# Kernel optimization log

Measured on AMD Instinct MI355X. Metric: run time of the kernel, lower is better.

The kernel has to match this reference:

```python
import jax, jax.numpy as jnp
import numpy as np

B, T = 128, 50
VOCAB, EMB_D, GRU_H = 10000, 200, 100
HEADS, AHID, THID = 8, 96, 96

def _conv(x, w, b, pad):
    y = jax.lax.conv_general_dilated(x, w, (1, 1), pad,
        dimension_numbers=('NCHW', 'OIHW', 'NCHW'))
    return y + b[None, :, None, None]

def _bn(x, g, b, m, v):
    s = jax.lax.rsqrt(v + 1e-5)
    return (x - m[None, :, None, None]) * (g * s)[None, :, None, None] + b[None, :, None, None]

def _maxpool(x):
    return jax.lax.reduce_window(x, -jnp.inf, jax.lax.max, (1, 1, 2, 2), (1, 1, 2, 2), 'VALID')

def _resize(x):
    # F.interpolate(mode='bilinear', align_corners=False) == half-pixel bilinear, no antialias
    return jax.image.resize(x, (x.shape[0], x.shape[1], 25, 156), 'bilinear', antialias=False)

def _audio_attn(x, wq, bq, wk, bk, wv, bv):
    # x: [B,96,H,W]; wq: [heads,96,96] == stacked per-head 1x1 convs
    Q = jnp.einsum('bchw,noc->bnohw', x, wq) + bq[None, :, :, None, None]
    K = jnp.einsum('bchw,noc->bnohw', x, wk) + bk[None, :, :, None, None]
    V = jnp.einsum('bchw,noc->bnohw', x, wv) + bv[None, :, :, None, None]
    # torch F.softmax with no dim on a 4D tensor defaults to dim=1 (channels) -> axis=2 here
    return jax.nn.softmax(Q * K, axis=2) * V  # [B,heads,96,H,W]

def _text_attn(o, wq, bq, wk, bk, wv, bv):
    # o: [N,100]; wq: [heads,96,100] == stacked per-head Linear layers
    Q = jnp.einsum('nd,hod->nho', o, wq) + bq[None]
    K = jnp.einsum('nd,hod->nho', o, wk) + bk[None]
    V = jnp.einsum('nd,hod->nho', o, wv) + bv[None]
    a = jax.nn.softmax(Q * K, axis=2) * V  # 2D softmax default dim=1 -> over feature axis
    return a.reshape(o.shape[0], -1)  # head-concat order == torch cat along dim=1

def _gru(xs, w_ih, w_hh, b_ih, b_hh):
    # xs: [T,B,200]; torch gate order r, z, n; b_hn applied inside r-gating
    def step(h, x):
        gi = x @ w_ih.T + b_ih
        gh = h @ w_hh.T + b_hh
        ir, iz, inew = jnp.split(gi, 3, axis=1)
        hr, hz, hnew = jnp.split(gh, 3, axis=1)
        r = jax.nn.sigmoid(ir + hr)
        z = jax.nn.sigmoid(iz + hz)
        n = jnp.tanh(inew + r * hnew)
        h2 = (1.0 - z) * n + z * h
        return h2, h2
    h0 = jnp.zeros((xs.shape[1], GRU_H), xs.dtype)
    hT, outs = jax.lax.scan(step, h0, xs)
    return outs, hT

def _forward(tokens, lengths, mfcc_t, mfcc_f, mfcc_c, w1a, b1a, g1a, be1a, m1a, v1a, w1b, b1b, g1b, be1b, m1b, v1b, w2, b2, g2, be2, m2, v2, w3, b3, g3, be3, m3, v3, w4, b4, g4, be4, m4, v4, wq_a1, bq_a1, wk_a1, bk_a1, wv_a1, bv_a1, wq_a2, bq_a2, wk_a2, bk_a2, wv_a2, bv_a2, emb, w_ih, w_hh, b_ih, b_hh, wq_t1, bq_t1, wk_t1, bk_t1, wv_t1, bv_t1, wq_t2, bq_t2, wk_t2, bk_t2, wv_t2, bv_t2, w_fa, b_fa, w_ft, b_ft, w_e, b_e):
    # --- audio CNN stem (eval-mode batchnorm; dropout off) ---
    xa = jax.nn.relu(_bn(_conv(mfcc_t, w1a, b1a, 'VALID'), g1a, be1a, m1a, v1a))
    xb = jax.nn.relu(_bn(_conv(mfcc_f, w1b, b1b, 'VALID'), g1b, be1b, m1b, v1b))
    # NOTE: original source reuses conv1b/bn1b for the third input (faithful to that)
    xc = jax.nn.relu(_bn(_conv(mfcc_c, w1b, b1b, 'VALID'), g1b, be1b, m1b, v1b))
    x = jnp.concatenate([_resize(xa), _resize(xb), _resize(xc)], axis=1)  # [B,24,25,156]
    x = _maxpool(jax.nn.relu(_bn(_conv(x, w2, b2, [(1, 1), (1, 1)]), g2, be2, m2, v2)))  # [B,32,12,78]
    x = _maxpool(jax.nn.relu(_bn(_conv(x, w3, b3, [(1, 1), (1, 1)]), g3, be3, m3, v3)))  # [B,64,6,39]
    x = jax.nn.relu(_bn(_conv(x, w4, b4, [(1, 1), (1, 1)]), g4, be4, m4, v4))            # [B,96,6,39]
    # --- two stacked per-head audio attentions, then per-head spatial GAP ---
    a1 = _audio_attn(x, wq_a1, bq_a1, wk_a1, bk_a1, wv_a1, bv_a1).mean(axis=(-2, -1))  # [B,8,96]
    a2 = _audio_attn(x, wq_a2, bq_a2, wk_a2, bk_a2, wv_a2, bv_a2).mean(axis=(-2, -1))
    # forward() slices heads along the height concat and GAPs -> per head [stage1 96, stage2 96]
    self_attn_audio = jnp.concatenate([a1, a2], axis=2).reshape(x.shape[0], -1)  # [B,1536]
    # --- text branch: embedding + GRU (all lengths == T -> pack/pad is identity) ---
    ex = jnp.swapaxes(emb[tokens], 0, 1)  # [T,B,200]
    outs, h = _gru(ex, w_ih, w_hh, b_ih, b_hh)  # h: [B,100]
    output = jnp.swapaxes(outs, 0, 1).reshape(-1, GRU_H)  # [B*T,100]
    t1 = _text_attn(output, wq_t1, bq_t1, wk_t1, bk_t1, wv_t1, bv_t1)
    t2 = _text_attn(output, wq_t2, bq_t2, wk_t2, bk_t2, wv_t2, bv_t2)
    self_attn_text = jnp.concatenate([t1, t2], axis=1).reshape(x.shape[0], T, -1).sum(axis=1)  # [B,1536]
    # --- cross-modal gated fusion ---
    x_gap = x.mean(axis=(-2, -1))  # [B,96]
    a_text = jax.nn.softmax(x_gap @ w_fa.T + b_fa, axis=1)   # [B,100]
    attn_text_based_audio = a_text * h                        # [B,100]
    a_audio = jax.nn.softmax(h @ w_ft.T + b_ft, axis=1)      # [B,96]
    attn_audio_based_text = a_audio * x_gap                   # [B,96]
    feat = jnp.concatenate([self_attn_audio, self_attn_text,
                            attn_audio_based_text, attn_text_based_audio], axis=1)  # [B,3268]
    return feat @ w_e.T + b_e  # [B,4] emotion logits

def setup_inputs() -> dict:
    key = jax.random.key(0)
    ks = iter(jax.random.split(key, 100))
    nrm = lambda s, sc=0.05: jax.random.normal(next(ks), s, jnp.float32) * sc
    uni = lambda s: jax.random.uniform(next(ks), s, jnp.float32) * 0.5 + 0.5
    d = {}
    d['mfcc_t'] = jax.random.normal(next(ks), (B, 1, 200, 40), jnp.float32)
    d['mfcc_f'] = jax.random.normal(next(ks), (B, 1, 200, 40), jnp.float32)
    d['mfcc_c'] = jax.random.normal(next(ks), (B, 1, 200, 40), jnp.float32)
    d['tokens'] = jax.random.randint(next(ks), (B, T), 0, VOCAB)
    d['lengths'] = jnp.full((B,), T, jnp.int32)
    def bnp(pre, c):
        d['g' + pre] = 1.0 + nrm((c,)); d['be' + pre] = nrm((c,))
        d['m' + pre] = nrm((c,)); d['v' + pre] = uni((c,))
    d['w1a'] = nrm((8, 1, 5, 2), 0.2); d['b1a'] = nrm((8,)); bnp('1a', 8)
    d['w1b'] = nrm((8, 1, 2, 6), 0.2); d['b1b'] = nrm((8,)); bnp('1b', 8)
    d['w2'] = nrm((32, 24, 3, 3), 0.1); d['b2'] = nrm((32,)); bnp('2', 32)
    d['w3'] = nrm((64, 32, 3, 3), 0.1); d['b3'] = nrm((64,)); bnp('3', 64)
    d['w4'] = nrm((96, 64, 3, 3), 0.08); d['b4'] = nrm((96,)); bnp('4', 96)
    for s in ('1', '2'):
        for p in ('q', 'k', 'v'):
            d['w%s_a%s' % (p, s)] = nrm((HEADS, 96, 96), 0.1)
            d['b%s_a%s' % (p, s)] = nrm((HEADS, 96))
    d['emb'] = nrm((VOCAB, EMB_D), 0.1)
    d['w_ih'] = nrm((3 * GRU_H, EMB_D), 0.1); d['w_hh'] = nrm((3 * GRU_H, GRU_H), 0.1)
    d['b_ih'] = nrm((3 * GRU_H,)); d['b_hh'] = nrm((3 * GRU_H,))
    for s in ('1', '2'):
        for p in ('q', 'k', 'v'):
            d['w%s_t%s' % (p, s)] = nrm((HEADS, THID, GRU_H), 0.1)
            d['b%s_t%s' % (p, s)] = nrm((HEADS, THID))
    d['w_fa'] = nrm((100, 96), 0.1); d['b_fa'] = nrm((100,))
    d['w_ft'] = nrm((96, 100), 0.1); d['b_ft'] = nrm((96,))
    d['w_e'] = nrm((4, 2 * HEADS * AHID + 2 * HEADS * THID + 96 + 100), 0.05); d['b_e'] = nrm((4,))
    return d

def reference(mfcc_t, mfcc_f, mfcc_c, tokens, lengths, w1a, b1a, g1a, be1a, m1a, v1a, w1b, b1b, g1b, be1b, m1b, v1b, w2, b2, g2, be2, m2, v2, w3, b3, g3, be3, m3, v3, w4, b4, g4, be4, m4, v4, wq_a1, bq_a1, wk_a1, bk_a1, wv_a1, bv_a1, wq_a2, bq_a2, wk_a2, bk_a2, wv_a2, bv_a2, emb, w_ih, w_hh, b_ih, b_hh, wq_t1, bq_t1, wk_t1, bk_t1, wv_t1, bv_t1, wq_t2, bq_t2, wk_t2, bk_t2, wv_t2, bv_t2, w_fa, b_fa, w_ft, b_ft, w_e, b_e):
    return _forward(tokens, lengths, mfcc_t, mfcc_f, mfcc_c, w1a, b1a, g1a, be1a, m1a, v1a, w1b, b1b, g1b, be1b, m1b, v1b, w2, b2, g2, be2, m2, v2, w3, b3, g3, be3, m3, v3, w4, b4, g4, be4, m4, v4, wq_a1, bq_a1, wk_a1, bk_a1, wv_a1, bv_a1, wq_a2, bq_a2, wk_a2, bk_a2, wv_a2, bv_a2, emb, w_ih, w_hh, b_ih, b_hh, wq_t1, bq_t1, wk_t1, bk_t1, wv_t1, bv_t1, wq_t2, bq_t2, wk_t2, bk_t2, wv_t2, bv_t2, w_fa, b_fa, w_ft, b_ft, w_e, b_e)
```

## Files before the change

### kernel.cpp

```cpp
#include <hip/hip_runtime.h>
#include <math.h>

static constexpr int kB = 128;
static constexpr int kT = 50;

struct TDesc { const float* src; float* dst; int O; int C; int total; };
struct TPack { TDesc d[15]; };
__global__ void k_transpose_pack(TPack p, float* __restrict__ za) {
    if (blockIdx.y == 15) {
        for (int i = blockIdx.x * 256 + threadIdx.x; i < 196608; i += 76800)
            za[i] = 0.f;
        return;
    }
    TDesc t = p.d[blockIdx.y];
    int idx = blockIdx.x * 256 + threadIdx.x;
    if (idx >= t.total) return;
    int o = idx % t.O; int r = idx / t.O; int c = r % t.C; int n = r / t.C;
    t.dst[idx] = t.src[((size_t)n * t.O + o) * t.C + c];
}

__global__ void __launch_bounds__(320) k_gi(const int* __restrict__ tokens,
        const float* __restrict__ emb, const float* __restrict__ w_ih,
        const float* __restrict__ b_ih, float* __restrict__ GI) {
    int r0 = blockIdx.x * 8;
    int tid = threadIdx.x;
    __shared__ float er[8][200];
    for (int e = tid; e < 1600; e += 320) {
        int r = e / 200, c = e - r * 200;
        er[r][c] = emb[(size_t)tokens[r0 + r] * 200 + c];
    }
    __syncthreads();
    if (tid < 300) {
        float acc[8];
        float bv = b_ih[tid];
        #pragma unroll
        for (int r = 0; r < 8; ++r) acc[r] = bv;
        for (int k4 = 0; k4 < 50; ++k4) {
            float4 w4 = *(const float4*)(w_ih + (size_t)tid * 200 + k4 * 4);
            #pragma unroll
            for (int r = 0; r < 8; ++r) {
                float4 x4 = *(const float4*)&er[r][k4 * 4];
                acc[r] += w4.x * x4.x + w4.y * x4.y + w4.z * x4.z + w4.w * x4.w;
            }
        }
        #pragma unroll
        for (int r = 0; r < 8; ++r)
            GI[(size_t)(r0 + r) * 300 + tid] = acc[r];
    }
}

__global__ void __launch_bounds__(256) k_fat_stem_gru(
    const float* __restrict__ mt, const float* __restrict__ mf,
    const float* __restrict__ mc,
    const float* __restrict__ w1a, const float* __restrict__ b1a,
    const float* __restrict__ g1a, const float* __restrict__ be1a,
    const float* __restrict__ m1a, const float* __restrict__ v1a,
    const float* __restrict__ w1b, const float* __restrict__ b1b,
    const float* __restrict__ g1b, const float* __restrict__ be1b,
    const float* __restrict__ m1b, const float* __restrict__ v1b,
    float* __restrict__ out, int total,
    const float* __restrict__ GI, const float* __restrict__ w_hh,
    const float* __restrict__ b_hh, float* __restrict__ outsT) {
    if (blockIdx.x < 128) {
        const int b = blockIdx.x, tid = threadIdx.x;
        __shared__ float hs[100];
        __shared__ float gH[300];
        const float bias0 = b_hh[tid];
        const float bias1 = (tid < 44) ? b_hh[256 + tid] : 0.f;
        if (tid < 100) hs[tid] = 0.f;
        __syncthreads();
        for (int t = 0; t < kT; ++t) {
            {
                float gh = bias0;
                const float* wr = w_hh + (size_t)tid * 100;
                #pragma unroll
                for (int k4 = 0; k4 < 25; ++k4) {
                    float4 w4 = *(const float4*)(wr + k4 * 4);
                    float4 h4 = *(const float4*)&hs[k4 * 4];
                    gh += w4.x * h4.x + w4.y * h4.y + w4.z * h4.z + w4.w * h4.w;
                }
                gH[tid] = gh;
            }
            if (tid < 44) {
                float gh = bias1;
                const float* wr = w_hh + (size_t)(256 + tid) * 100;
                #pragma unroll
                for (int k4 = 0; k4 < 25; ++k4) {
                    float4 w4 = *(const float4*)(wr + k4 * 4);
                    float4 h4 = *(const float4*)&hs[k4 * 4];
                    gh += w4.x * h4.x + w4.y * h4.y + w4.z * h4.z + w4.w * h4.w;
                }
                gH[256 + tid] = gh;
            }
            __syncthreads();
            if (tid < 100) {
                const float* gi = GI + ((size_t)b * kT + t) * 300;
                float r = 1.f / (1.f + expf(-(gi[tid] + gH[tid])));
                float z = 1.f / (1.f + expf(-(gi[100 + tid] + gH[100 + tid])));
                float nn = tanhf(gi[200 + tid] + r * gH[200 + tid]);
                float h2 = (1.f - z) * nn + z * hs[tid];
                hs[tid] = h2;
                outsT[((size_t)b * 100 + tid) * kT + t] = h2;
            }
            __syncthreads();
        }
        return;
    }
    int idx = (blockIdx.x - 128) * 256 + threadIdx.x;
    if (idx >= total) return;
    int ox = idx % 156; int t = idx / 156;
    int oy = t % 25; t /= 25;
    int ch = t % 24; int b = t / 24;
    int grp = ch >> 3, c = ch & 7;
    const float* src; int Hc, Wc;
    const float *wb, *cb, *g, *be, *m, *v;
    if (grp == 0) { src = mt; Hc = 196; Wc = 39; wb = w1a + c * 10;
                    cb = b1a; g = g1a; be = be1a; m = m1a; v = v1a; }
    else          { src = (grp == 1 ? mf : mc); Hc = 199; Wc = 35; wb = w1b + c * 12;
                    cb = b1b; g = g1b; be = be1b; m = m1b; v = v1b; }
    float s = g[c] * rsqrtf(v[c] + 1e-5f);
    float bias = (cb[c] - m[c]) * s + be[c];
    float sy = (oy + 0.5f) * ((float)Hc / 25.f) - 0.5f;
    float sx = (ox + 0.5f) * ((float)Wc / 156.f) - 0.5f;
    float fy0 = floorf(sy), fx0 = floorf(sx);
    float fy = sy - fy0, fx = sx - fx0;
    int y0 = (int)fy0, x0 = (int)fx0;
    int y0c = min(max(y0, 0), Hc - 1), y1c = min(max(y0 + 1, 0), Hc - 1);
    int x0c = min(max(x0, 0), Wc - 1), x1c = min(max(x0 + 1, 0), Wc - 1);
    bool xs = (x1c == x0c), ys = (y1c == y0c);
    const float* p = src + (size_t)b * 8000;
    float t00, t01, t10, t11;
    if (grp == 0) {
        float W[6][3];
        #pragma unroll
        for (int r = 0; r < 6; ++r) {
            int rr = min(y0c + r, 199);
            #pragma unroll
            for (int cc = 0; cc < 3; ++cc)
                W[r][cc] = p[rr * 40 + min(x0c + cc, 39)];
        }
        float a00 = 0.f, a01 = 0.f, a10 = 0.f, a11 = 0.f;
        #pragma unroll
        for (int ky = 0; ky < 5; ++ky)
            #pragma unroll
            for (int kx = 0; kx < 2; ++kx) {
                float wv = wb[ky * 2 + kx];
                a00 += W[ky][kx] * wv;     a01 += W[ky][kx + 1] * wv;
                a10 += W[ky + 1][kx] * wv; a11 += W[ky + 1][kx + 1] * wv;
            }
        t00 = a00;
        t01 = xs ? a00 : a01;
        t10 = ys ? a00 : a10;
        t11 = xs ? (ys ? a00 : a10) : (ys ? a01 : a11);
    } else {
        float W[3][7];
        #pragma unroll
        for (int r = 0; r < 3; ++r) {
            int rr = min(y0c + r, 199);
            #pragma unroll
            for (int cc = 0; cc < 7; ++cc)
                W[r][cc] = p[rr * 40 + min(x0c + cc, 39)];
        }
        float a00 = 0.f, a01 = 0.f, a10 = 0.f, a11 = 0.f;
        #pragma unroll
        for (int ky = 0; ky < 2; ++ky)
            #pragma unroll
            for (int kx = 0; kx < 6; ++kx) {
                float wv = wb[ky * 6 + kx];
                a00 += W[ky][kx] * wv;     a01 += W[ky][kx + 1] * wv;
                a10 += W[ky + 1][kx] * wv; a11 += W[ky + 1][kx + 1] * wv;
            }
        t00 = a00;
        t01 = xs ? a00 : a01;
        t10 = ys ? a00 : a10;
        t11 = xs ? (ys ? a00 : a10) : (ys ? a01 : a11);
    }
    float r00 = fmaxf(t00 * s + bias, 0.f), r01 = fmaxf(t01 * s + bias, 0.f);
    float r10 = fmaxf(t10 * s + bias, 0.f), r11 = fmaxf(t11 * s + bias, 0.f);
    out[idx] = r00 * (1.f - fy) * (1.f - fx) + r01 * (1.f - fy) * fx
             + r10 * fy * (1.f - fx) + r11 * fy * fx;
}

template<int CIN, int CI_T, int H, int W, int ROWS, int NPX>
__global__ void __launch_bounds__(256) k_conv3x3_tiled(
    const float* __restrict__ in, const float* __restrict__ wT,
    const float* __restrict__ cb, const float* __restrict__ g,
    const float* __restrict__ be, const float* __restrict__ m,
    const float* __restrict__ v, float* __restrict__ out, int COUT) {
    constexpr int WP = W + 2;
    constexpr int RP = ROWS + 2;
    constexpr int STAGE = CI_T * RP * WP;
    __shared__ float sx[STAGE];
    __shared__ float sw[CI_T * 9 * 8];
    const int b = blockIdx.x, rt = blockIdx.y, oc0 = blockIdx.z * 8;
    const int row0 = rt * ROWS;
    const int tid = threadIdx.x;

    int off[NPX]; bool val[NPX];
    #pragma unroll
    for (int j = 0; j < NPX; ++j) {
        int px = tid + j * 256;
        int oy = px / W, ox = px - oy * W;
        bool ok = (px < ROWS * W) && (row0 + oy < H);
        val[j] = ok;
        off[j] = ok ? (oy * WP + ox) : 0;
    }

    float acc[NPX][8];
    #pragma unroll
    for (int j = 0; j < NPX; ++j)
        #pragma unroll
        for (int o = 0; o < 8; ++o) acc[j][o] = 0.f;

    for (int c0 = 0; c0 < CIN; c0 += CI_T) {
        __syncthreads();
        for (int e = tid; e < STAGE; e += 256) {
            int ci = e / (RP * WP);
            int rem = e - ci * RP * WP;
            int r = rem / WP;
            int xx = rem - r * WP;
            int iy = row0 - 1 + r;
            int ix = xx - 1;
            float vv = 0.f;
            if (iy >= 0 && iy < H && ix >= 0 && ix < W)
                vv = in[((size_t)(b * CIN + c0 + ci) * H + iy) * W + ix];
            sx[e] = vv;
        }
        for (int e = tid; e < CI_T * 9 * 8; e += 256) {
            int rk = e >> 3;
            int o = e & 7;
            sw[e] = wT[((size_t)c0 * 9 + rk) * COUT + oc0 + o];
        }
        __syncthreads();
        #pragma unroll 1
        for (int cl = 0; cl < CI_T; ++cl) {
            const float* sxc = sx + cl * RP * WP;
            #pragma unroll
            for (int k = 0; k < 9; ++k) {
                const int ky = k / 3, kx = k % 3;
                const float4 wa = *(const float4*)(sw + (cl * 9 + k) * 8);
                const float4 wb = *(const float4*)(sw + (cl * 9 + k) * 8 + 4);
                #pragma unroll
                for (int j = 0; j < NPX; ++j) {
                    float xv = sxc[off[j] + ky * WP + kx];
                    acc[j][0] += xv * wa.x; acc[j][1] += xv * wa.y;
                    acc[j][2] += xv * wa.z; acc[j][3] += xv * wa.w;
                    acc[j][4] += xv * wb.x; acc[j][5] += xv * wb.y;
                    acc[j][6] += xv * wb.z; acc[j][7] += xv * wb.w;
                }
            }
        }
    }
    float sc[8], bi[8];
    #pragma unroll
    for (int o = 0; o < 8; ++o) {
        float s = g[oc0 + o] * rsqrtf(v[oc0 + o] + 1e-5f);
        sc[o] = s; bi[o] = (cb[oc0 + o] - m[oc0 + o]) * s + be[oc0 + o];
    }
    #pragma unroll
    for (int j = 0; j < NPX; ++j) if (val[j]) {
        int px = tid + j * 256;
        int oy = row0 + px / W, ox = px % W;
        #pragma unroll
        for (int o = 0; o < 8; ++o)
            out[((size_t)(b * COUT + oc0 + o) * H + oy) * W + ox] =
                fmaxf(acc[j][o] * sc[o] + bi[o], 0.f);
    }
}

__global__ void k_maxpool(const float* __restrict__ in, float* __restrict__ out,
                          int C, int Hin, int Win, int Hout, int Wout, int total) {
    int idx = blockIdx.x * blockDim.x + threadIdx.x;
    if (idx >= total) return;
    int ox = idx % Wout; int t = idx / Wout;
    int oy = t % Hout; t /= Hout;
    int c = t % C; int b = t / C;
    const float* p = in + ((size_t)(b * C + c) * Hin + 2 * oy) * Win + 2 * ox;
    float m0 = fmaxf(p[0], p[1]);
    float m1 = fmaxf(p[Win], p[Win + 1]);
    out[idx] = fmaxf(m0, m1);
}

__global__ void __launch_bounds__(256) k_xgap(const float* __restrict__ x,
                                              float* __restrict__ xgap) {
    int b = blockIdx.x, tid = threadIdx.x;
    int wave = tid >> 6, lane = tid & 63;
    for (int c = wave; c < 96; c += 4) {
        const float* row = x + ((size_t)b * 96 + c) * 234;
        float s = 0.f;
        for (int p = lane; p < 234; p += 64) s += row[p];
        #pragma unroll
        for (int off = 1; off < 64; off <<= 1) s += __shfl_xor(s, off);
        if (lane == 0) xgap[b * 96 + c] = s * (1.f / 234.f);
    }
}

__global__ void __launch_bounds__(256, 2) k_audio_attn(
    const float* __restrict__ x,
    const float* __restrict__ wq1, const float* __restrict__ bq1,
    const float* __restrict__ wk1, const float* __restrict__ bk1,
    const float* __restrict__ wv1, const float* __restrict__ bv1,
    const float* __restrict__ wq2, const float* __restrict__ bq2,
    const float* __restrict__ wk2, const float* __restrict__ bk2,
    const float* __restrict__ wv2, const float* __restrict__ bv2,
    float* __restrict__ afeat) {
    const int b = blockIdx.x >> 1, pt = blockIdx.x & 1;
    const int n = blockIdx.y, stage = blockIdx.z;
    const float* wq = (stage ? wq2 : wq1) + n * 9216;
    const float* wk = (stage ? wk2 : wk1) + n * 9216;
    const float* wv = (stage ? wv2 : wv1) + n * 9216;
    const float* bqn = (stage ? bq2 : bq1) + n * 96;
    const float* bkn = (stage ? bk2 : bk1) + n * 96;
    const float* bvn = (stage ? bv2 : bv1) + n * 96;
    const int tid = threadIdx.x;
    const int to = tid >> 4, tpg = tid & 15;
    const int ob = to * 6;
    const int pA = tpg * 4;
    const int p0 = pt * 128;

    __shared__ float sxc[16 * 128];
    __shared__ float sw[4608];
    float* sred = sw;

    const float* xb = x + (size_t)b * (96 * 234) + p0;

    float qa[6][8], ka[6][8], va[6][8];
    #pragma unroll
    for (int j = 0; j < 6; ++j) {
        float bq_ = bqn[ob + j], bk_ = bkn[ob + j], bv_ = bvn[ob + j];
        #pragma unroll
        for (int i = 0; i < 8; ++i) { qa[j][i] = bq_; ka[j][i] = bk_; va[j][i] = bv_; }
    }

    for (int c0 = 0; c0 < 96; c0 += 16) {
        __syncthreads();
        {
            #pragma unroll
            for (int it = 0; it < 4; ++it) {
                int e2 = tid + it * 256;
                int r = e2 >> 6, c2 = (e2 & 63) * 2;
                float2 v = make_float2(0.f, 0.f);
                if (p0 + c2 < 234) v = *(const float2*)(xb + (c0 + r) * 234 + c2);
                *(float2*)(sxc + r * 128 + c2) = v;
            }
        }
        for (int e4 = tid; e4 < 1152; e4 += 256) {
            int mat = (e4 >= 768) ? 2 : (e4 >= 384 ? 1 : 0);
            int r4 = e4 - mat * 384;
            const float* wsrc = (mat == 0) ? wq : (mat == 1 ? wk : wv);
            *(float4*)(sw + mat * 1536 + r4 * 4) = *(const float4*)(wsrc + c0 * 96 + r4 * 4);
        }
        __syncthreads();
        #pragma unroll 2
        for (int cc = 0; cc < 16; ++cc) {
            float4 xa = *(const float4*)(sxc + cc * 128 + pA);
            float4 xc = *(const float4*)(sxc + cc * 128 + 64 + pA);
            const float* wr = sw + cc * 96 + ob;
            float2 q01 = *(const float2*)(wr);
            float2 q23 = *(const float2*)(wr + 2);
            float2 q45 = *(const float2*)(wr + 4);
            float2 k01 = *(const float2*)(wr + 1536);
            float2 k23 = *(const float2*)(wr + 1538);
            float2 k45 = *(const float2*)(wr + 1540);
            float2 v01 = *(const float2*)(wr + 3072);
            float2 v23 = *(const float2*)(wr + 3074);
            float2 v45 = *(const float2*)(wr + 3076);
            float wqv[6] = {q01.x, q01.y, q23.x, q23.y, q45.x, q45.y};
            float wkv[6] = {k01.x, k01.y, k23.x, k23.y, k45.x, k45.y};
            float wvv[6] = {v01.x, v01.y, v23.x, v23.y, v45.x, v45.y};
            #pragma unroll
            for (int j = 0; j < 6; ++j) {
                qa[j][0] += wqv[j] * xa.x; qa[j][1] += wqv[j] * xa.y;
                qa[j][2] += wqv[j] * xa.z; qa[j][3] += wqv[j] * xa.w;
                qa[j][4] += wqv[j] * xc.x; qa[j][5] += wqv[j] * xc.y;
                qa[j][6] += wqv[j] * xc.z; qa[j][7] += wqv[j] * xc.w;
                ka[j][0] += wkv[j] * xa.x; ka[j][1] += wkv[j] * xa.y;
                ka[j][2] += wkv[j] * xa.z; ka[j][3] += wkv[j] * xa.w;
                ka[j][4] += wkv[j] * xc.x; ka[j][5] += wkv[j] * xc.y;
                ka[j][6] += wkv[j] * xc.z; ka[j][7] += wkv[j] * xc.w;
                va[j][0] += wvv[j] * xa.x; va[j][1] += wvv[j] * xa.y;
                va[j][2] += wvv[j] * xa.z; va[j][3] += wvv[j] * xa.w;
                va[j][4] += wvv[j] * xc.x; va[j][5] += wvv[j] * xc.y;
                va[j][6] += wvv[j] * xc.z; va[j][7] += wvv[j] * xc.w;
            }
        }
    }

    int col[8];
    #pragma unroll
    for (int i = 0; i < 4; ++i) { col[i] = pA + i; col[4 + i] = 64 + pA + i; }

    float pmx[8];
    #pragma unroll
    for (int i = 0; i < 8; ++i) pmx[i] = -1e30f;
    #pragma unroll
    for (int j = 0; j < 6; ++j)
        #pragma unroll
        for (int i = 0; i < 8; ++i) {
            float sv = qa[j][i] * ka[j][i];
            qa[j][i] = sv;
            pmx[i] = fmaxf(pmx[i], sv);
        }
    __syncthreads();
    #pragma unroll
    for (int i = 0; i < 8; ++i) sred[to * 128 + col[i]] = pmx[i];
    __syncthreads();
    float m_[8];
    #pragma unroll
    for (int i = 0; i < 8; ++i) {
        float mm = -1e30f;
        for (int t = 0; t < 16; ++t) mm = fmaxf(mm, sred[t * 128 + col[i]]);
        m_[i] = mm;
    }
    __syncthreads();
    float z[8];
    #pragma unroll
    for (int i = 0; i < 8; ++i) z[i] = 0.f;
    #pragma unroll
    for (int j = 0; j < 6; ++j)
        #pragma unroll
        for (int i = 0; i < 8; ++i) {
            float e = __expf(qa[j][i] - m_[i]);
            qa[j][i] = e;
            z[i] += e;
        }
    #pragma unroll
    for (int i = 0; i < 8; ++i) sred[to * 128 + col[i]] = z[i];
    __syncthreads();
    float rz[8];
    #pragma unroll
    for (int i = 0; i < 8; ++i) {
        float zs = 0.f;
        for (int t = 0; t < 16; ++t) zs += sred[t * 128 + col[i]];
        rz[i] = (p0 + col[i] < 234) ? 1.f / zs : 0.f;
    }
    __syncthreads();
    #pragma unroll
    for (int j = 0; j < 6; ++j) {
        float po = 0.f;
        #pragma unroll
        for (int i = 0; i < 8; ++i) po += qa[j][i] * rz[i] * va[j][i];
        sred[(ob + j) * 16 + tpg] = po;
    }
    __syncthreads();
    if (tid < 96) {
        float ssum = 0.f;
        #pragma unroll
        for (int t = 0; t < 16; ++t) ssum += sred[tid * 16 + t];
        atomicAdd(afeat + b * 1536 + n * 192 + stage * 96 + tid, ssum * (1.f / 234.f));
    }
}

__global__ void __launch_bounds__(256, 2) k_text_attn(
    const float* __restrict__ outsT,
    const float* __restrict__ wq1, const float* __restrict__ bq1,
    const float* __restrict__ wk1, const float* __restrict__ bk1,
    const float* __restrict__ wv1, const float* __restrict__ bv1,
    const float* __restrict__ wq2, const float* __restrict__ bq2,
    const float* __restrict__ wk2, const float* __restrict__ bk2,
    const float* __restrict__ wv2, const float* __restrict__ bv2,
    float* __restrict__ tfeat) {
    const int b = blockIdx.x, stage = blockIdx.y, n = blockIdx.z;
    const float* wq = (stage ? wq2 : wq1) + n * 9600;
    const float* wk = (stage ? wk2 : wk1) + n * 9600;
    const float* wv = (stage ? wv2 : wv1) + n * 9600;
    const float* bqn = (stage ? bq2 : bq1) + n * 96;
    const float* bkn = (stage ? bk2 : bk1) + n * 96;
    const float* bvn = (stage ? bv2 : bv1) + n * 96;
    const int tid = threadIdx.x;
    const int to = tid >> 4, tpg = tid & 15;
    const int ob = to * 6;
    const int tA = tpg * 4;

    __shared__ float sxc[20 * 64];
    __shared__ float sw[5760];
    float* sred = sw;

    const float* xb = outsT + (size_t)b * (100 * kT);

    float qa[6][4], ka[6][4], va[6][4];
    #pragma unroll
    for (int j = 0; j < 6; ++j) {
        float bq_ = bqn[ob + j], bk_ = bkn[ob + j], bv_ = bvn[ob + j];
        #pragma unroll
        for (int i = 0; i < 4; ++i) { qa[j][i] = bq_; ka[j][i] = bk_; va[j][i] = bv_; }
    }

    for (int c0 = 0; c0 < 100; c0 += 20) {
        __syncthreads();
        for (int e = tid; e < 1280; e += 256) {
            int r = e >> 6, tt = e & 63;
            sxc[e] = (tt < kT) ? xb[(c0 + r) * kT + tt] : 0.f;
        }
        for (int e4 = tid; e4 < 1440; e4 += 256) {
            int mat = (e4 >= 960) ? 2 : (e4 >= 480 ? 1 : 0);
            int r4 = e4 - mat * 480;
            const float* wsrc = (mat == 0) ? wq : (mat == 1 ? wk : wv);
            *(float4*)(sw + mat * 1920 + r4 * 4) = *(const float4*)(wsrc + c0 * 96 + r4 * 4);
        }
        __syncthreads();
        #pragma unroll 4
        for (int cc = 0; cc < 20; ++cc) {
            float4 xa = *(const float4*)(sxc + cc * 64 + tA);
            const float* wr = sw + cc * 96 + ob;
            float2 q01 = *(const float2*)(wr);
            float2 q23 = *(const float2*)(wr + 2);
            float2 q45 = *(const float2*)(wr + 4);
            float2 k01 = *(const float2*)(wr + 1920);
            float2 k23 = *(const float2*)(wr + 1922);
            float2 k45 = *(const float2*)(wr + 1924);
            float2 v01 = *(const float2*)(wr + 3840);
            float2 v23 = *(const float2*)(wr + 3842);
            float2 v45 = *(const float2*)(wr + 3844);
            float wqv[6] = {q01.x, q01.y, q23.x, q23.y, q45.x, q45.y};
            float wkv[6] = {k01.x, k01.y, k23.x, k23.y, k45.x, k45.y};
            float wvv[6] = {v01.x, v01.y, v23.x, v23.y, v45.x, v45.y};
            #pragma unroll
            for (int j = 0; j < 6; ++j) {
                qa[j][0] += wqv[j] * xa.x; qa[j][1] += wqv[j] * xa.y;
                qa[j][2] += wqv[j] * xa.z; qa[j][3] += wqv[j] * xa.w;
                ka[j][0] += wkv[j] * xa.x; ka[j][1] += wkv[j] * xa.y;
                ka[j][2] += wkv[j] * xa.z; ka[j][3] += wkv[j] * xa.w;
                va[j][0] += wvv[j] * xa.x; va[j][1] += wvv[j] * xa.y;
                va[j][2] += wvv[j] * xa.z; va[j][3] += wvv[j] * xa.w;
            }
        }
    }

    float pmx[4] = {-1e30f, -1e30f, -1e30f, -1e30f};
    #pragma unroll
    for (int j = 0; j < 6; ++j)
        #pragma unroll
        for (int i = 0; i < 4; ++i) {
            float sv = qa[j][i] * ka[j][i];
            qa[j][i] = sv;
            pmx[i] = fmaxf(pmx[i], sv);
        }
    __syncthreads();
    #pragma unroll
    for (int i = 0; i < 4; ++i) sred[to * 64 + tA + i] = pmx[i];
    __syncthreads();
    float m_[4];
    #pragma unroll
    for (int i = 0; i < 4; ++i) {
        float mm = -1e30f;
        for (int t = 0; t < 16; ++t) mm = fmaxf(mm, sred[t * 64 + tA + i]);
        m_[i] = mm;
    }
    __syncthreads();
    float z[4] = {0.f, 0.f, 0.f, 0.f};
    #pragma unroll
    for (int j = 0; j < 6; ++j)
        #pragma unroll
        for (int i = 0; i < 4; ++i) {
            float e = __expf(qa[j][i] - m_[i]);
            qa[j][i] = e;
            z[i] += e;
        }
    #pragma unroll
    for (int i = 0; i < 4; ++i) sred[to * 64 + tA + i] = z[i];
    __syncthreads();
    float rz[4];
    #pragma unroll
    for (int i = 0; i < 4; ++i) {
        float zs = 0.f;
        for (int t = 0; t < 16; ++t) zs += sred[t * 64 + tA + i];
        rz[i] = (tA + i < kT) ? 1.f / zs : 0.f;
    }
    __syncthreads();
    #pragma unroll
    for (int j = 0; j < 6; ++j) {
        float po = qa[j][0] * rz[0] * va[j][0]
                 + qa[j][1] * rz[1] * va[j][1]
                 + qa[j][2] * rz[2] * va[j][2]
                 + qa[j][3] * rz[3] * va[j][3];
        sred[(ob + j) * 16 + tpg] = po;
    }
    __syncthreads();
    if (tid < 96) {
        float ssum = 0.f;
        #pragma unroll
        for (int t = 0; t < 16; ++t) ssum += sred[tid * 16 + t];
        tfeat[b * 1536 + stage * 768 + n * 96 + tid] = ssum;
    }
}

__global__ void __launch_bounds__(128) k_final(const float* __restrict__ xgap,
    const float* __restrict__ outsT, const float* __restrict__ afeat,
    const float* __restrict__ tfeat,
    const float* __restrict__ w_fa, const float* __restrict__ b_fa,
    const float* __restrict__ w_ft, const float* __restrict__ b_ft,
    const float* __restrict__ w_e, const float* __restrict__ b_e,
    float* __restrict__ out) {
    int b = blockIdx.x; int tid = threadIdx.x;
    __shared__ float xg[96], hv[100], st[100], sa[96], aat[96], atba[100];
    __shared__ float redm[2], reds[2];
    if (tid < 96) xg[tid] = xgap[b * 96 + tid];
    if (tid < 100) hv[tid] = outsT[((size_t)b * 100 + tid) * kT + (kT - 1)];
    __syncthreads();
    if (tid < 100) {
        float acc = b_fa[tid];
        const float* wr = w_fa + tid * 96;
        for (int c = 0; c < 96; ++c) acc += wr[c] * xg[c];
        st[tid] = acc;
    }
    if (tid < 96) {
        float acc = b_ft[tid];
        const float* wr = w_ft + tid * 100;
        for (int c = 0; c < 100; ++c) acc += wr[c] * hv[c];
        sa[tid] = acc;
    }
    __syncthreads();
    if (tid == 0) {
        float mxv = -1e30f; for (int i = 0; i < 100; ++i) mxv = fmaxf(mxv, st[i]);
        float s = 0.f; for (int i = 0; i < 100; ++i) s += expf(st[i] - mxv);
        redm[0] = mxv; reds[0] = s;
    }
    if (tid == 1) {
        float mxv = -1e30f; for (int i = 0; i < 96; ++i) mxv = fmaxf(mxv, sa[i]);
        float s = 0.f; for (int i = 0; i < 96; ++i) s += expf(sa[i] - mxv);
        redm[1] = mxv; reds[1] = s;
    }
    __syncthreads();
    if (tid < 100) atba[tid] = expf(st[tid] - redm[0]) / reds[0] * hv[tid];
    if (tid < 96)  aat[tid]  = expf(sa[tid] - redm[1]) / reds[1] * xg[tid];
    __syncthreads();
    float a0 = 0.f, a1 = 0.f, a2 = 0.f, a3 = 0.f;
    for (int col = tid; col < 3268; col += 128) {
        float f;
        if (col < 1536)      f = afeat[b * 1536 + col];
        else if (col < 3072) f = tfeat[b * 1536 + col - 1536];
        else if (col < 3168) f = aat[col - 3072];
        else                 f = atba[col - 3168];
        a0 += w_e[col] * f;            a1 += w_e[3268 + col] * f;
        a2 += w_e[2 * 3268 + col] * f; a3 += w_e[3 * 3268 + col] * f;
    }
    __shared__ float r4[4][128];
    r4[0][tid] = a0; r4[1][tid] = a1; r4[2][tid] = a2; r4[3][tid] = a3;
    __syncthreads();
    if (tid < 4) {
        float s = 0.f;
        for (int i = 0; i < 128; ++i) s += r4[tid][i];
        out[b * 4 + tid] = s + b_e[tid];
    }
}

extern "C" void kernel_launch(void* const* d_in, const int* in_sizes, int n_in,
                              void* d_out, int out_size, void* d_ws, size_t ws_size,
                              hipStream_t stream) {
    (void)in_sizes; (void)n_in; (void)out_size; (void)ws_size;
    const float* mfcc_t = (const float*)d_in[0];
    const float* mfcc_f = (const float*)d_in[1];
    const float* mfcc_c = (const float*)d_in[2];
    const int*   tokens = (const int*)d_in[3];
    const float *w1a = (const float*)d_in[5],  *b1a = (const float*)d_in[6],
                *g1a = (const float*)d_in[7],  *be1a = (const float*)d_in[8],
                *m1a = (const float*)d_in[9],  *v1a = (const float*)d_in[10];
    const float *w1b = (const float*)d_in[11], *b1b = (const float*)d_in[12],
                *g1b = (const float*)d_in[13], *be1b = (const float*)d_in[14],
                *m1b = (const float*)d_in[15], *v1b = (const float*)d_in[16];
    const float *w2 = (const float*)d_in[17], *b2 = (const float*)d_in[18],
                *g2 = (const float*)d_in[19], *be2 = (const float*)d_in[20],
                *m2 = (const float*)d_in[21], *v2 = (const float*)d_in[22];
    const float *w3 = (const float*)d_in[23], *b3 = (const float*)d_in[24],
                *g3 = (const float*)d_in[25], *be3 = (const float*)d_in[26],
                *m3 = (const float*)d_in[27], *v3 = (const float*)d_in[28];
    const float *w4 = (const float*)d_in[29], *b4 = (const float*)d_in[30],
                *g4 = (const float*)d_in[31], *be4 = (const float*)d_in[32],
                *m4 = (const float*)d_in[33], *v4 = (const float*)d_in[34];
    const float *wq_a1 = (const float*)d_in[35], *bq_a1 = (const float*)d_in[36],
                *wk_a1 = (const float*)d_in[37], *bk_a1 = (const float*)d_in[38],
                *wv_a1 = (const float*)d_in[39], *bv_a1 = (const float*)d_in[40];
    const float *wq_a2 = (const float*)d_in[41], *bq_a2 = (const float*)d_in[42],
                *wk_a2 = (const float*)d_in[43], *bk_a2 = (const float*)d_in[44],
                *wv_a2 = (const float*)d_in[45], *bv_a2 = (const float*)d_in[46];
    const float *emb  = (const float*)d_in[47];
    const float *w_ih = (const float*)d_in[48], *w_hh = (const float*)d_in[49],
                *b_ih = (const float*)d_in[50], *b_hh = (const float*)d_in[51];
    const float *wq_t1 = (const float*)d_in[52], *bq_t1 = (const float*)d_in[53],
                *wk_t1 = (const float*)d_in[54], *bk_t1 = (const float*)d_in[55],
                *wv_t1 = (const float*)d_in[56], *bv_t1 = (const float*)d_in[57];
    const float *wq_t2 = (const float*)d_in[58], *bq_t2 = (const float*)d_in[59],
                *wk_t2 = (const float*)d_in[60], *bk_t2 = (const float*)d_in[61],
                *wv_t2 = (const float*)d_in[62], *bv_t2 = (const float*)d_in[63];
    const float *w_fa = (const float*)d_in[64], *b_fa = (const float*)d_in[65],
                *w_ft = (const float*)d_in[66], *b_ft = (const float*)d_in[67],
                *w_e  = (const float*)d_in[68], *b_e  = (const float*)d_in[69];

    float* ws = (float*)d_ws;
    const size_t Z0 = 0;
    const size_t Z1 = 22091776ull;
    const size_t OUTS  = 34072576ull;
    const size_t AFEAT = 34712576ull;
    const size_t TFEAT = 34909184ull;
    const size_t XGAP  = 35105792ull;
    const size_t WT    = 35118080ull;
    float* GI = ws + Z0;
    float* X1 = ws + Z1;
    float* C2 = ws + Z0;  float* P2 = ws + Z1;
    float* C3 = ws + Z0;  float* P3 = ws + Z1;
    float* X4 = ws + Z0;
    float* outsT = ws + OUTS;
    float* afeat = ws + AFEAT;
    float* tfeat = ws + TFEAT;
    float* xgap  = ws + XGAP;
    float* wqa1t = ws + WT;
    float* wka1t = wqa1t + 73728; float* wva1t = wka1t + 73728;
    float* wqa2t = wva1t + 73728; float* wka2t = wqa2t + 73728; float* wva2t = wka2t + 73728;
    float* wqt1t = wva2t + 73728;
    float* wkt1t = wqt1t + 76800; float* wvt1t = wkt1t + 76800;
    float* wqt2t = wvt1t + 76800; float* wkt2t = wqt2t + 76800; float* wvt2t = wkt2t + 76800;
    float* wT2 = tfeat;
    float* wT3 = tfeat + 6912;
    float* wT4 = tfeat + 25344;

    TPack tp;
    tp.d[0]  = {wq_a1, wqa1t, 96, 96, 73728};
    tp.d[1]  = {wk_a1, wka1t, 96, 96, 73728};
    tp.d[2]  = {wv_a1, wva1t, 96, 96, 73728};
    tp.d[3]  = {wq_a2, wqa2t, 96, 96, 73728};
    tp.d[4]  = {wk_a2, wka2t, 96, 96, 73728};
    tp.d[5]  = {wv_a2, wva2t, 96, 96, 73728};
    tp.d[6]  = {w2, wT2, 32, 216, 6912};
    tp.d[7]  = {w3, wT3, 64, 288, 18432};
    tp.d[8]  = {w4, wT4, 96, 576, 55296};
    tp.d[9]  = {wq_t1, wqt1t, 96, 100, 76800};
    tp.d[10] = {wk_t1, wkt1t, 96, 100, 76800};
    tp.d[11] = {wv_t1, wvt1t, 96, 100, 76800};
    tp.d[12] = {wq_t2, wqt2t, 96, 100, 76800};
    tp.d[13] = {wk_t2, wkt2t, 96, 100, 76800};
    tp.d[14] = {wv_t2, wvt2t, 96, 100, 76800};
    k_transpose_pack<<<dim3(300, 16), 256, 0, stream>>>(tp, afeat);

    k_gi<<<kB * kT / 8, 320, 0, stream>>>(tokens, emb, w_ih, b_ih, GI);

    k_fat_stem_gru<<<46928, 256, 0, stream>>>(mfcc_t, mfcc_f, mfcc_c,
        w1a, b1a, g1a, be1a, m1a, v1a,
        w1b, b1b, g1b, be1b, m1b, v1b, X1, 11980800,
        GI, w_hh, b_hh, outsT);

    k_conv3x3_tiled<24, 8, 25, 156, 9, 6><<<dim3(128, 3, 4), 256, 0, stream>>>(
        X1, wT2, b2, g2, be2, m2, v2, C2, 32);
    k_maxpool<<<14976, 256, 0, stream>>>(C2, P2, 32, 25, 156, 12, 78, 3833856);
    k_conv3x3_tiled<32, 8, 12, 78, 12, 4><<<dim3(128, 1, 8), 256, 0, stream>>>(
        P2, wT3, b3, g3, be3, m3, v3, C3, 64);
    k_maxpool<<<7488, 256, 0, stream>>>(C3, P3, 64, 12, 78, 6, 39, 1916928);
    k_conv3x3_tiled<64, 16, 6, 39, 6, 1><<<dim3(128, 1, 12), 256, 0, stream>>>(
        P3, wT4, b4, g4, be4, m4, v4, X4, 96);

    k_text_attn<<<dim3(kB, 2, 8), 256, 0, stream>>>(outsT,
        wqt1t, bq_t1, wkt1t, bk_t1, wvt1t, bv_t1,
        wqt2t, bq_t2, wkt2t, bk_t2, wvt2t, bv_t2, tfeat);
    k_xgap<<<kB, 256, 0, stream>>>(X4, xgap);

    k_audio_attn<<<dim3(kB * 2, 8, 2), 256, 0, stream>>>(X4,
        wqa1t, bq_a1, wka1t, bk_a1, wva1t, bv_a1,
        wqa2t, bq_a2, wka2t, bk_a2, wva2t, bv_a2, afeat);

    k_final<<<kB, 128, 0, stream>>>(xgap, outsT, afeat, tfeat,
                                    w_fa, b_fa, w_ft, b_ft, w_e, b_e, (float*)d_out);
}
```

Before: 1.346 ms.

## Fuse maxpool into conv epilogue and compute 16 output channels per block

The 3x3 conv kernel now computes 16 output channels per block instead of 8, so each staged input tile is reused across twice as many channels. For the first two convs, the ReLU output is staged in shared memory one channel at a time and 2x2 max-pooled before being written. This removes the two separate maxpool launches and the full-resolution intermediate writes and reads. In exchange it doubles the accumulator registers, halves the grid, and adds per-channel barriers in the pooled epilogue.

```diff
diff --git a/kernel.cpp b/kernel.cpp
--- a/kernel.cpp
+++ b/kernel.cpp
@@ -181,18 +181,18 @@
              + r10 * fy * (1.f - fx) + r11 * fy * fx;
 }
 
-template<int CIN, int CI_T, int H, int W, int ROWS, int NPX>
-__global__ void __launch_bounds__(256) k_conv3x3_tiled(
+template<int CIN, int CI_T, int H, int W, int ROWS, int NPX, bool POOL>
+__global__ void __launch_bounds__(256) k_conv16(
     const float* __restrict__ in, const float* __restrict__ wT,
     const float* __restrict__ cb, const float* __restrict__ g,
     const float* __restrict__ be, const float* __restrict__ m,
-    const float* __restrict__ v, float* __restrict__ out, int COUT) {
+    const float* __restrict__ v, float* __restrict__ out, int COUT, int PHT) {
     constexpr int WP = W + 2;
     constexpr int RP = ROWS + 2;
     constexpr int STAGE = CI_T * RP * WP;
     __shared__ float sx[STAGE];
-    __shared__ float sw[CI_T * 9 * 8];
-    const int b = blockIdx.x, rt = blockIdx.y, oc0 = blockIdx.z * 8;
+    __shared__ float sw[CI_T * 9 * 16];
+    const int b = blockIdx.x, rt = blockIdx.y, oc0 = blockIdx.z * 16;
     const int row0 = rt * ROWS;
     const int tid = threadIdx.x;
 
@@ -206,11 +206,11 @@
         off[j] = ok ? (oy * WP + ox) : 0;
     }
 
-    float acc[NPX][8];
+    float acc[NPX][16];
     #pragma unroll
     for (int j = 0; j < NPX; ++j)
         #pragma unroll
-        for (int o = 0; o < 8; ++o) acc[j][o] = 0.f;
+        for (int o = 0; o < 16; ++o) acc[j][o] = 0.f;
 
     for (int c0 = 0; c0 < CIN; c0 += CI_T) {
         __syncthreads();
@@ -226,9 +226,9 @@
                 vv = in[((size_t)(b * CIN + c0 + ci) * H + iy) * W + ix];
             sx[e] = vv;
         }
-        for (int e = tid; e < CI_T * 9 * 8; e += 256) {
-            int rk = e >> 3;
-            int o = e & 7;
+        for (int e = tid; e < CI_T * 9 * 16; e += 256) {
+            int rk = e >> 4;
+            int o = e & 15;
             sw[e] = wT[((size_t)c0 * 9 + rk) * COUT + oc0 + o];
         }
         __syncthreads();
@@ -238,47 +238,61 @@
             #pragma unroll
             for (int k = 0; k < 9; ++k) {
                 const int ky = k / 3, kx = k % 3;
-                const float4 wa = *(const float4*)(sw + (cl * 9 + k) * 8);
-                const float4 wb = *(const float4*)(sw + (cl * 9 + k) * 8 + 4);
+                const float* wb_ = sw + (cl * 9 + k) * 16;
+                const float4 wa = *(const float4*)(wb_);
+                const float4 wb2 = *(const float4*)(wb_ + 4);
+                const float4 wc = *(const float4*)(wb_ + 8);
+                const float4 wd = *(const float4*)(wb_ + 12);
                 #pragma unroll
                 for (int j = 0; j < NPX; ++j) {
                     float xv = sxc[off[j] + ky * WP + kx];
-                    acc[j][0] += xv * wa.x; acc[j][1] += xv * wa.y;
-                    acc[j][2] += xv * wa.z; acc[j][3] += xv * wa.w;
-                    acc[j][4] += xv * wb.x; acc[j][5] += xv * wb.y;
-                    acc[j][6] += xv * wb.z; acc[j][7] += xv * wb.w;
+                    acc[j][0]  += xv * wa.x;  acc[j][1]  += xv * wa.y;
+                    acc[j][2]  += xv * wa.z;  acc[j][3]  += xv * wa.w;
+                    acc[j][4]  += xv * wb2.x; acc[j][5]  += xv * wb2.y;
+                    acc[j][6]  += xv * wb2.z; acc[j][7]  += xv * wb2.w;
+                    acc[j][8]  += xv * wc.x;  acc[j][9]  += xv * wc.y;
+                    acc[j][10] += xv * wc.z;  acc[j][11] += xv * wc.w;
+                    acc[j][12] += xv * wd.x;  acc[j][13] += xv * wd.y;
+                    acc[j][14] += xv * wd.z;  acc[j][15] += xv * wd.w;
                 }
             }
         }
     }
-    float sc[8], bi[8];
-    #pragma unroll
-    for (int o = 0; o < 8; ++o) {
+    float sc[16], bi[16];
+    #pragma unroll
+    for (int o = 0; o < 16; ++o) {
         float s = g[oc0 + o] * rsqrtf(v[oc0 + o] + 1e-5f);
         sc[o] = s; bi[o] = (cb[oc0 + o] - m[oc0 + o]) * s + be[oc0 + o];
     }
-    #pragma unroll
-    for (int j = 0; j < NPX; ++j) if (val[j]) {
-        int px = tid + j * 256;
-        int oy = row0 + px / W, ox = px % W;
-        #pragma unroll
-        for (int o = 0; o < 8; ++o)
-            out[((size_t)(b * COUT + oc0 + o) * H + oy) * W + ox] =
-                fmaxf(acc[j][o] * sc[o] + bi[o], 0.f);
-    }
-}
-
-__global__ void k_maxpool(const float* __restrict__ in, float* __restrict__ out,
-                          int C, int Hin, int Win, int Hout, int Wout, int total) {
-    int idx = blockIdx.x * blockDim.x + threadIdx.x;
-    if (idx >= total) return;
-    int ox = idx % Wout; int t = idx / Wout;
-    int oy = t % Hout; t /= Hout;
-    int c = t % C; int b = t / C;
-    const float* p = in + ((size_t)(b * C + c) * Hin + 2 * oy) * Win + 2 * ox;
-    float m0 = fmaxf(p[0], p[1]);
-    float m1 = fmaxf(p[Win], p[Win + 1]);
-    out[idx] = fmaxf(m0, m1);
+    if (!POOL) {
+        #pragma unroll
+        for (int j = 0; j < NPX; ++j) if (val[j]) {
+            int px = tid + j * 256;
+            int oy = row0 + px / W, ox = px % W;
+            #pragma unroll
+            for (int o = 0; o < 16; ++o)
+                out[((size_t)(b * COUT + oc0 + o) * H + oy) * W + ox] =
+                    fmaxf(acc[j][o] * sc[o] + bi[o], 0.f);
+        }
+    } else {
+        constexpr int PH = ROWS / 2, PW = W / 2, PT = PH * PW;
+        const int prow0 = rt * PH;
+        for (int o = 0; o < 16; ++o) {
+            __syncthreads();
+            #pragma unroll
+            for (int j = 0; j < NPX; ++j) if (val[j]) {
+                int px = tid + j * 256;
+                sx[px] = fmaxf(acc[j][o] * sc[o] + bi[o], 0.f);
+            }
+            __syncthreads();
+            for (int e = tid; e < PT; e += 256) {
+                int py = e / PW, pxl = e - py * PW;
+                const float* r0 = sx + (2 * py) * W + 2 * pxl;
+                float mv = fmaxf(fmaxf(r0[0], r0[1]), fmaxf(r0[W], r0[W + 1]));
+                out[((size_t)(b * COUT + oc0 + o) * PHT + prow0 + py) * PW + pxl] = mv;
+            }
+        }
+    }
 }
 
 __global__ void __launch_bounds__(256) k_xgap(const float* __restrict__ x,
@@ -697,8 +711,8 @@
     const size_t WT    = 35118080ull;
     float* GI = ws + Z0;
     float* X1 = ws + Z1;
-    float* C2 = ws + Z0;  float* P2 = ws + Z1;
-    float* C3 = ws + Z0;  float* P3 = ws + Z1;
+    float* P2 = ws + Z0;
+    float* P3 = ws + Z1;
     float* X4 = ws + Z0;
     float* outsT = ws + OUTS;
     float* afeat = ws + AFEAT;
@@ -739,14 +753,12 @@
         w1b, b1b, g1b, be1b, m1b, v1b, X1, 11980800,
         GI, w_hh, b_hh, outsT);
 
-    k_conv3x3_tiled<24, 8, 25, 156, 9, 6><<<dim3(128, 3, 4), 256, 0, stream>>>(
-        X1, wT2, b2, g2, be2, m2, v2, C2, 32);
-    k_maxpool<<<14976, 256, 0, stream>>>(C2, P2, 32, 25, 156, 12, 78, 3833856);
-    k_conv3x3_tiled<32, 8, 12, 78, 12, 4><<<dim3(128, 1, 8), 256, 0, stream>>>(
-        P2, wT3, b3, g3, be3, m3, v3, C3, 64);
-    k_maxpool<<<7488, 256, 0, stream>>>(C3, P3, 64, 12, 78, 6, 39, 1916928);
-    k_conv3x3_tiled<64, 16, 6, 39, 6, 1><<<dim3(128, 1, 12), 256, 0, stream>>>(
-        P3, wT4, b4, g4, be4, m4, v4, X4, 96);
+    k_conv16<24, 8, 25, 156, 8, 5, true><<<dim3(128, 3, 2), 256, 0, stream>>>(
+        X1, wT2, b2, g2, be2, m2, v2, P2, 32, 12);
+    k_conv16<32, 8, 12, 78, 12, 4, true><<<dim3(128, 1, 4), 256, 0, stream>>>(
+        P2, wT3, b3, g3, be3, m3, v3, P3, 64, 6);
+    k_conv16<64, 16, 6, 39, 6, 1, false><<<dim3(128, 1, 6), 256, 0, stream>>>(
+        P3, wT4, b4, g4, be4, m4, v4, X4, 96, 0);
 
     k_text_attn<<<dim3(kB, 2, 8), 256, 0, stream>>>(outsT,
         wqt1t, bq_t1, wkt1t, bk_t1, wvt1t, bv_t1,
```

Result: faster. 1.299 ms (-3.5%).
